# Kernel optimization log

Hardware: AMD Instinct MI355X
Metric: run time of the kernel (lower is better)

Reference implementation:

```python
import jax, jax.numpy as jnp
import numpy as np

EPS = 1e-06
H_BW = 0.5  # bandwidth h


def setup_inputs() -> dict:
    key = jax.random.key(0)
    k1, k2 = jax.random.split(key)
    N, C, H, W = 8, 256, 64, 64
    x = jax.random.normal(k1, (N, C, H, W), dtype=jnp.float32)
    y = jax.random.normal(k2, (N, C, H, W), dtype=jnp.float32)
    return {"x": x, "y": y}


def reference(x, y):
    N, C, _H, _W = x.shape
    # mean over W, H, then batch -> per-channel mean, shape (1, C, 1, 1)
    y_mu = y.mean(axis=3).mean(axis=2).mean(axis=0).reshape(1, C, 1, 1)
    x_c = x - y_mu
    y_c = y - y_mu
    # L2-normalize over channel dim (matches torch.norm without eps)
    x_n = x_c / jnp.linalg.norm(x_c, axis=1, keepdims=True)
    y_n = y_c / jnp.linalg.norm(y_c, axis=1, keepdims=True)
    x_n = x_n.reshape(N, C, -1)  # (N, C, HW)
    y_n = y_n.reshape(N, C, -1)
    # cosine similarity: (N, HW, HW)
    cosine_sim = jnp.einsum('nci,ncj->nij', x_n, y_n)
    d = 1.0 - cosine_sim
    d_min = jnp.min(d, axis=2, keepdims=True)
    d_tilde = d / (d_min + EPS)
    w = jnp.exp((1.0 - d_tilde) / H_BW)
    ccx_ij = w / jnp.sum(w, axis=2, keepdims=True)
    ccx = jnp.mean(jnp.max(ccx_ij, axis=1), axis=1)  # (N,)
    return jnp.mean(-jnp.log(ccx + EPS))
```

## Files before the change

### kernel.cpp

```cpp
#include <hip/hip_runtime.h>
#include <hip/hip_bf16.h>

#define HW 4096
#define CC 256
#define NBATCH 8
#define EPSF 1e-6f

typedef __attribute__((ext_vector_type(4))) float floatx4;
typedef long long llong;

#define GLDS(g, l) __builtin_amdgcn_global_load_lds( \
    (const __attribute__((address_space(1))) void*)(const void*)(g), \
    (__attribute__((address_space(3))) void*)(void*)(l), 16, 0, 0)

__device__ __forceinline__ unsigned fkey(float f){
    unsigned u = __float_as_uint(f);
    return (u & 0x80000000u) ? ~u : (u | 0x80000000u);
}
__device__ __forceinline__ float fdec(unsigned k){
    unsigned u = (k & 0x80000000u) ? (k ^ 0x80000000u) : ~k;
    return __uint_as_float(u);
}
__device__ __forceinline__ unsigned short f2bf(float f){
    unsigned u = __float_as_uint(f);
    u += 0x7FFFu + ((u >> 16) & 1);
    return (unsigned short)(u >> 16);
}

__global__ __launch_bounds__(256) void kmean(const float* __restrict__ y,
                                             float* __restrict__ ymu){
    const int c = blockIdx.x;
    const int t = threadIdx.x;
    float s = 0.f;
    for(int n = 0; n < NBATCH; n++){
        const float4* p = reinterpret_cast<const float4*>(y + ((size_t)n*CC + c)*HW);
        #pragma unroll
        for(int i = 0; i < 4; i++){
            float4 v = p[i*256 + t];
            s += (v.x + v.y) + (v.z + v.w);
        }
    }
    __shared__ float red[256];
    red[t] = s; __syncthreads();
    for(int off = 128; off > 0; off >>= 1){
        if(t < off) red[t] += red[t+off];
        __syncthreads();
    }
    if(t == 0) ymu[c] = red[0] * (1.0f/((float)NBATCH*HW));
}

#define TROW 264
__global__ __launch_bounds__(256) void knorm(const float* __restrict__ x,
                                             const float* __restrict__ y,
                                             const float* __restrict__ ymu,
                                             unsigned char* __restrict__ xF,
                                             unsigned char* __restrict__ yF,
                                             unsigned* __restrict__ dmink,
                                             float* __restrict__ rowsum,
                                             unsigned* __restrict__ colmaxk){
    __shared__ __align__(16) unsigned short tile[64*TROW];
    __shared__ float invn[64];
    __shared__ float partial[4][64];
    __shared__ float smu[CC];
    const int t   = threadIdx.x;
    const int hw0 = blockIdx.x * 64;
    const int n   = blockIdx.y;
    if(t < 64){
        size_t g = (size_t)n*HW + hw0 + t;
        dmink[g] = 0xFFFFFFFFu;
        rowsum[g] = 0.f;
        colmaxk[g] = 0u;
    }
    for(int c = t; c < CC; c += 256) smu[c] = ymu[c];
    const int hwl = t & 63;
    const int cch = t >> 6;
    for(int which = 0; which < 2; which++){
        const float* __restrict__ src = which ? y : x;
        unsigned char* __restrict__ dst = which ? yF : xF;
        __syncthreads();
        float ss = 0.f;
        for(int cc = 0; cc < 64; cc++){
            int c = cch*64 + cc;
            float v = src[((size_t)n*CC + c)*HW + hw0 + hwl] - smu[c];
            ss += v*v;
            tile[hwl*TROW + c] = f2bf(v);
        }
        partial[cch][hwl] = ss;
        __syncthreads();
        if(t < 64){
            float s = partial[0][t]+partial[1][t]+partial[2][t]+partial[3][t];
            invn[t] = rsqrtf(s);
        }
        __syncthreads();
        size_t base = ((size_t)n << 20) + (size_t)(hw0 >> 4)*4096;
        #pragma unroll
        for(int v4 = 0; v4 < 4; v4++){
            int g  = v4*256 + t;
            int it = g >> 8;
            int kt = (g >> 5) & 7;
            int qq = (g >> 3) & 3;
            int u  = g & 7;
            int r0 = it*16 + u*2;
            unsigned w[4];
            #pragma unroll
            for(int rr = 0; rr < 2; rr++){
                int r = r0 + rr;
                float inv = invn[r];
                const unsigned* lp = reinterpret_cast<const unsigned*>(&tile[r*TROW + kt*32 + qq*8]);
                float f[8];
                #pragma unroll
                for(int w2 = 0; w2 < 4; w2++){
                    unsigned uu = lp[w2];
                    f[2*w2]   = __uint_as_float((uu & 0xFFFFu) << 16) * inv;
                    f[2*w2+1] = __uint_as_float(uu & 0xFFFF0000u) * inv;
                }
                unsigned wa = 0, wb = 0;
                wa = __builtin_amdgcn_cvt_pk_fp8_f32(f[0], f[1], wa, false);
                wa = __builtin_amdgcn_cvt_pk_fp8_f32(f[2], f[3], wa, true);
                wb = __builtin_amdgcn_cvt_pk_fp8_f32(f[4], f[5], wb, false);
                wb = __builtin_amdgcn_cvt_pk_fp8_f32(f[6], f[7], wb, true);
                w[2*rr] = wa; w[2*rr+1] = wb;
            }
            uint4 ov; ov.x=w[0]; ov.y=w[1]; ov.z=w[2]; ov.w=w[3];
            *reinterpret_cast<uint4*>(dst + base + it*4096 + kt*512 + qq*128 + u*16) = ov;
        }
    }
}

template<int MODE>
__global__ __launch_bounds__(256, 2) void ksweep(
        const unsigned char* __restrict__ xF,
        const unsigned char* __restrict__ yF,
        unsigned* __restrict__ dmink,
        float* __restrict__ rowsum,
        unsigned* __restrict__ colmaxk){
    __shared__ __align__(16) unsigned char Bs[2][16384];
    __shared__ __align__(16) float bbS[4][128];
    const int t    = threadIdx.x;
    const int lane = t & 63;
    const int wave = t >> 6;
    const int q    = lane >> 4;
    const int l15  = lane & 15;
    const int bid  = blockIdx.x;
    const int n    = bid & 7;
    const int rem  = bid >> 3;
    const int ip   = rem & 7;
    const int jq   = rem >> 3;
    const size_t nb8 = (size_t)n << 20;
    const size_t nbw = (size_t)n * HW;
    const int iw   = ip*512 + wave*128;
    const unsigned char* Ax = xF + nb8 + (size_t)(iw >> 4)*4096 + (size_t)lane*8;
    const unsigned char* Yb = yF + nb8 + (size_t)jq*131072;

    llong af[8][8];
    #pragma unroll
    for(int ti = 0; ti < 8; ti++)
        #pragma unroll
        for(int kt = 0; kt < 8; kt++)
            af[ti][kt] = *reinterpret_cast<const llong*>(Ax + ti*4096 + kt*512);

    float sc[8][4];
    if(MODE >= 1){
        #pragma unroll
        for(int ti = 0; ti < 8; ti++)
            #pragma unroll
            for(int r = 0; r < 4; r++){
                size_t g = nbw + iw + ti*16 + q*4 + r;
                sc[ti][r] = 2.f / (fdec(dmink[g]) + EPSF);
            }
    }
    if(MODE == 2){
        #pragma unroll
        for(int rr = 0; rr < 2; rr++){
            int row = lane*2 + rr;
            bbS[wave][row] = 2.f - __logf(rowsum[nbw + iw + row]);
        }
    }
    float racc[8][4];
    #pragma unroll
    for(int ti = 0; ti < 8; ti++)
        #pragma unroll
        for(int r = 0; r < 4; r++) racc[ti][r] = (MODE == 0) ? -3e38f : 0.f;

    #pragma unroll
    for(int p = 0; p < 4; p++){
        int c = wave*4 + p;
        GLDS(Yb + c*1024 + (size_t)lane*16, &Bs[0][c*1024]);
    }
    __syncthreads();

    #pragma unroll 1
    for(int ss = 0; ss < 8; ss++){
        {
            const unsigned char* src = Yb + (size_t)(ss+1)*16384;
            unsigned char* dstb = Bs[(ss+1)&1];
            #pragma unroll
            for(int p = 0; p < 4; p++){
                int c = wave*4 + p;
                GLDS(src + c*1024 + (size_t)lane*16, &dstb[c*1024]);
            }
        }
        #pragma unroll 1
        for(int u = 0; u < 4; u++){
            const unsigned char* B = &Bs[ss&1][u*4096];
            const int js = ss*4 + u;
            floatx4 acc[8];
            #pragma unroll
            for(int a = 0; a < 8; a++) acc[a] = (floatx4){0.f,0.f,0.f,0.f};
            #pragma unroll
            for(int kt = 0; kt < 8; kt++){
                llong b = *reinterpret_cast<const llong*>(B + kt*512 + lane*8);
                #pragma unroll
                for(int ti = 0; ti < 8; ti++)
                    acc[ti] = __builtin_amdgcn_mfma_f32_16x16x32_fp8_fp8(
                                  af[ti][kt], b, acc[ti], 0, 0, 0);
            }
            if(MODE == 0){
                #pragma unroll
                for(int ti = 0; ti < 8; ti++)
                    #pragma unroll
                    for(int r = 0; r < 4; r++)
                        racc[ti][r] = fmaxf(racc[ti][r], acc[ti][r]);
            } else if(MODE == 1){
                #pragma unroll
                for(int ti = 0; ti < 8; ti++)
                    #pragma unroll
                    for(int r = 0; r < 4; r++)
                        racc[ti][r] += __expf(fmaf(acc[ti][r] - 1.f, sc[ti][r], 2.f));
            } else {
                float a = -3e38f;
                #pragma unroll
                for(int ti = 0; ti < 8; ti++){
                    const floatx4 bb4 = *reinterpret_cast<const floatx4*>(&bbS[wave][ti*16 + q*4]);
                    #pragma unroll
                    for(int r = 0; r < 4; r++)
                        a = fmaxf(a, fmaf(acc[ti][r] - 1.f, sc[ti][r], bb4[r]));
                }
                a = fmaxf(a, __shfl_xor(a, 16));
                a = fmaxf(a, __shfl_xor(a, 32));
                if(lane < 16)
                    atomicMax(&colmaxk[nbw + jq*512 + js*16 + l15], fkey(__expf(a)));
            }
        }
        __syncthreads();
    }

    if(MODE == 0){
        #pragma unroll
        for(int ti = 0; ti < 8; ti++)
            #pragma unroll
            for(int r = 0; r < 4; r++){
                float v = racc[ti][r];
                v = fmaxf(v, __shfl_xor(v, 1));
                v = fmaxf(v, __shfl_xor(v, 2));
                v = fmaxf(v, __shfl_xor(v, 4));
                v = fmaxf(v, __shfl_xor(v, 8));
                if(l15 == 0)
                    atomicMin(&dmink[nbw + iw + ti*16 + q*4 + r], fkey(1.f - v));
            }
    } else if(MODE == 1){
        #pragma unroll
        for(int ti = 0; ti < 8; ti++)
            #pragma unroll
            for(int r = 0; r < 4; r++){
                float v = racc[ti][r];
                v += __shfl_xor(v, 1);
                v += __shfl_xor(v, 2);
                v += __shfl_xor(v, 4);
                v += __shfl_xor(v, 8);
                if(l15 == 0)
                    atomicAdd(&rowsum[nbw + iw + ti*16 + q*4 + r], v);
            }
    }
}

__global__ __launch_bounds__(256) void kpart(const unsigned* __restrict__ colmaxk,
                                             float* __restrict__ part){
    __shared__ float red[256];
    const int t = threadIdx.x;
    const int n = blockIdx.x;
    float s = 0.f;
    for(int j = t; j < HW; j += 256) s += fdec(colmaxk[(size_t)n*HW + j]);
    red[t] = s; __syncthreads();
    for(int off = 128; off > 0; off >>= 1){
        if(t < off) red[t] += red[t+off];
        __syncthreads();
    }
    if(t == 0) part[n] = -logf(red[0]*(1.0f/HW) + EPSF);
}

__global__ __launch_bounds__(64) void kfin(const float* __restrict__ part,
                                           float* __restrict__ out){
    const int t = threadIdx.x;
    float v = (t < NBATCH) ? part[t] : 0.f;
    v += __shfl_xor(v, 1);
    v += __shfl_xor(v, 2);
    v += __shfl_xor(v, 4);
    if(t == 0) out[0] = v * (1.0f/NBATCH);
}

extern "C" void kernel_launch(void* const* d_in, const int* in_sizes, int n_in,
                              void* d_out, int out_size, void* d_ws, size_t ws_size,
                              hipStream_t stream){
    const float* x = (const float*)d_in[0];
    const float* y = (const float*)d_in[1];
    float* out = (float*)d_out;
    char* ws = (char*)d_ws;

    float* ymu = (float*)ws;
    size_t off = 1024;
    unsigned char* xF = (unsigned char*)(ws + off); off += (size_t)NBATCH << 20;
    unsigned char* yF = (unsigned char*)(ws + off); off += ((size_t)NBATCH << 20) + (512<<10);
    unsigned* dmink   = (unsigned*)(ws + off);      off += (size_t)NBATCH*HW*4;
    float* rowsum     = (float*)(ws + off);         off += (size_t)NBATCH*HW*4;
    unsigned* colmaxk = (unsigned*)(ws + off);      off += (size_t)NBATCH*HW*4;
    float* part       = (float*)(ws + off);         off += 64;

    kmean<<<dim3(CC), dim3(256), 0, stream>>>(y, ymu);
    knorm<<<dim3(HW/64, NBATCH), dim3(256), 0, stream>>>(x, y, ymu, xF, yF,
                                                         dmink, rowsum, colmaxk);
    ksweep<0><<<dim3(512), dim3(256), 0, stream>>>(xF, yF, dmink, rowsum, colmaxk);
    ksweep<1><<<dim3(512), dim3(256), 0, stream>>>(xF, yF, dmink, rowsum, colmaxk);
    ksweep<2><<<dim3(512), dim3(256), 0, stream>>>(xF, yF, dmink, rowsum, colmaxk);
    kpart<<<dim3(NBATCH), dim3(256), 0, stream>>>(colmaxk, part);
    kfin<<<dim3(1), dim3(64), 0, stream>>>(part, out);
}
```

Before: 267.6 us.

## Use scaled 16x16x128 FP8 MFMA and move per-row scales to LDS

Replaces the eight 16x16x32 FP8 MFMAs per tile with two MX-scaled 16x16x128 f8f6f4 MFMAs, using unit exponent scales. This regroups the A and B operand fragments into 8-wide int vectors with a new lane-to-K mapping. Per-row scale factors move from registers into shared memory to free VGPRs, at the cost of extra LDS reads in the epilogue. The K-permutation must match on A and B for correctness, and the scale constant must encode a factor of one.

```diff
diff --git a/kernel.cpp b/kernel.cpp
--- a/kernel.cpp
+++ b/kernel.cpp
@@ -5,8 +5,10 @@
 #define CC 256
 #define NBATCH 8
 #define EPSF 1e-6f
+#define SCL1 0x7F7F7F7F
 
 typedef __attribute__((ext_vector_type(4))) float floatx4;
+typedef __attribute__((ext_vector_type(8))) int intx8;
 typedef long long llong;
 
 #define GLDS(g, l) __builtin_amdgcn_global_load_lds( \
@@ -127,6 +129,8 @@
     }
 }
 
+union U8 { intx8 v; llong d[4]; };
+
 template<int MODE>
 __global__ __launch_bounds__(256, 2) void ksweep(
         const unsigned char* __restrict__ xF,
@@ -135,6 +139,7 @@
         float* __restrict__ rowsum,
         unsigned* __restrict__ colmaxk){
     __shared__ __align__(16) unsigned char Bs[2][16384];
+    __shared__ __align__(16) float scS[4][128];
     __shared__ __align__(16) float bbS[4][128];
     const int t    = threadIdx.x;
     const int lane = t & 63;
@@ -149,31 +154,25 @@
     const size_t nb8 = (size_t)n << 20;
     const size_t nbw = (size_t)n * HW;
     const int iw   = ip*512 + wave*128;
-    const unsigned char* Ax = xF + nb8 + (size_t)(iw >> 4)*4096 + (size_t)lane*8;
+    const unsigned char* Ax = xF + nb8 + (size_t)(iw >> 4)*4096 + q*512 + l15*8;
     const unsigned char* Yb = yF + nb8 + (size_t)jq*131072;
 
-    llong af[8][8];
+    U8 af0[8], af1[8];
     #pragma unroll
     for(int ti = 0; ti < 8; ti++)
         #pragma unroll
-        for(int kt = 0; kt < 8; kt++)
-            af[ti][kt] = *reinterpret_cast<const llong*>(Ax + ti*4096 + kt*512);
-
-    float sc[8][4];
+        for(int qq = 0; qq < 4; qq++){
+            af0[ti].d[qq] = *reinterpret_cast<const llong*>(Ax + ti*4096 + qq*128);
+            af1[ti].d[qq] = *reinterpret_cast<const llong*>(Ax + ti*4096 + 2048 + qq*128);
+        }
+
     if(MODE >= 1){
-        #pragma unroll
-        for(int ti = 0; ti < 8; ti++)
-            #pragma unroll
-            for(int r = 0; r < 4; r++){
-                size_t g = nbw + iw + ti*16 + q*4 + r;
-                sc[ti][r] = 2.f / (fdec(dmink[g]) + EPSF);
-            }
-    }
-    if(MODE == 2){
         #pragma unroll
         for(int rr = 0; rr < 2; rr++){
             int row = lane*2 + rr;
-            bbS[wave][row] = 2.f - __logf(rowsum[nbw + iw + row]);
+            size_t g = nbw + iw + row;
+            scS[wave][row] = 2.f / (fdec(dmink[g]) + EPSF);
+            if(MODE == 2) bbS[wave][row] = 2.f - __logf(rowsum[g]);
         }
     }
     float racc[8][4];
@@ -202,18 +201,23 @@
         }
         #pragma unroll 1
         for(int u = 0; u < 4; u++){
-            const unsigned char* B = &Bs[ss&1][u*4096];
+            const unsigned char* Bq = &Bs[ss&1][u*4096] + q*512 + l15*8;
             const int js = ss*4 + u;
+            U8 b0, b1;
+            #pragma unroll
+            for(int qq = 0; qq < 4; qq++){
+                b0.d[qq] = *reinterpret_cast<const llong*>(Bq + qq*128);
+                b1.d[qq] = *reinterpret_cast<const llong*>(Bq + 2048 + qq*128);
+            }
             floatx4 acc[8];
             #pragma unroll
             for(int a = 0; a < 8; a++) acc[a] = (floatx4){0.f,0.f,0.f,0.f};
             #pragma unroll
-            for(int kt = 0; kt < 8; kt++){
-                llong b = *reinterpret_cast<const llong*>(B + kt*512 + lane*8);
-                #pragma unroll
-                for(int ti = 0; ti < 8; ti++)
-                    acc[ti] = __builtin_amdgcn_mfma_f32_16x16x32_fp8_fp8(
-                                  af[ti][kt], b, acc[ti], 0, 0, 0);
+            for(int ti = 0; ti < 8; ti++){
+                acc[ti] = __builtin_amdgcn_mfma_scale_f32_16x16x128_f8f6f4(
+                              af0[ti].v, b0.v, acc[ti], 0, 0, 0, SCL1, 0, SCL1);
+                acc[ti] = __builtin_amdgcn_mfma_scale_f32_16x16x128_f8f6f4(
+                              af1[ti].v, b1.v, acc[ti], 0, 0, 0, SCL1, 0, SCL1);
             }
             if(MODE == 0){
                 #pragma unroll
@@ -223,18 +227,21 @@
                         racc[ti][r] = fmaxf(racc[ti][r], acc[ti][r]);
             } else if(MODE == 1){
                 #pragma unroll
-                for(int ti = 0; ti < 8; ti++)
+                for(int ti = 0; ti < 8; ti++){
+                    const floatx4 sc4 = *reinterpret_cast<const floatx4*>(&scS[wave][ti*16 + q*4]);
                     #pragma unroll
                     for(int r = 0; r < 4; r++)
-                        racc[ti][r] += __expf(fmaf(acc[ti][r] - 1.f, sc[ti][r], 2.f));
+                        racc[ti][r] += __expf(fmaf(acc[ti][r] - 1.f, sc4[r], 2.f));
+                }
             } else {
                 float a = -3e38f;
                 #pragma unroll
                 for(int ti = 0; ti < 8; ti++){
+                    const floatx4 sc4 = *reinterpret_cast<const floatx4*>(&scS[wave][ti*16 + q*4]);
                     const floatx4 bb4 = *reinterpret_cast<const floatx4*>(&bbS[wave][ti*16 + q*4]);
                     #pragma unroll
                     for(int r = 0; r < 4; r++)
-                        a = fmaxf(a, fmaf(acc[ti][r] - 1.f, sc[ti][r], bb4[r]));
+                        a = fmaxf(a, fmaf(acc[ti][r] - 1.f, sc4[r], bb4[r]));
                 }
                 a = fmaxf(a, __shfl_xor(a, 16));
                 a = fmaxf(a, __shfl_xor(a, 32));
```

After: 233.3 us. 12.8% less time.
